# Performance work log

Measured on AMD Instinct MI355X. Metric: run time of the kernel, lower is better.

The kernel has to match this reference:

```python
import jax, jax.numpy as jnp
from jax import lax
import numpy as np
import math

B = 2; H = 64; W = 64; HW = H * W
CIN = 128; CH = 64          # in_chans, in_chans//2
E = 192; DEPTH = 2          # embed_dim, depth
DIN = 384; DST = 4; DTR = 12; KC = 4   # d_inner, d_state, dt_rank, d_conv
NC = 9
SAMPLE = HW // 2            # round(h*w*self_ratio), self_ratio=0.5
LE = HW - SAMPLE            # number of mask==0 (easy) tokens per row


def setup_inputs() -> dict:
    key = jax.random.key(0)
    ks = jax.random.split(key, 16)
    rn = lambda k, s, sc: jax.random.normal(k, s, jnp.float32) * sc
    return {
        'x': rn(ks[0], (B, CIN, H, W), 1.0),
        'head_id': 0,
        'sp_w': rn(ks[1], (1, CH, 1, 1), 1.0 / math.sqrt(CH)),
        'sp_b': jnp.zeros((1,), jnp.float32),
        'c0_w': rn(ks[2], (E, CIN, 1, 1), 1.0 / math.sqrt(CIN)),
        'c0_b': jnp.zeros((E,), jnp.float32),
        'blk_norm_w': jnp.ones((DEPTH, E), jnp.float32),
        'blk_conv_w': rn(ks[3], (DEPTH, E, E, 3, 3), 1.0 / math.sqrt(9 * E)),
        'blk_conv_b': jnp.zeros((DEPTH, E), jnp.float32),
        'm_in_w': rn(ks[4], (DEPTH, 2 * DIN, E), 1.0 / math.sqrt(E)),
        'm_conv_w': rn(ks[5], (DEPTH, DIN, KC), 1.0 / math.sqrt(KC)),
        'm_conv_b': jnp.zeros((DEPTH, DIN), jnp.float32),
        'm_x_w': rn(ks[6], (DEPTH, DTR + 2 * DST, DIN), 1.0 / math.sqrt(DIN)),
        'm_dt_w': rn(ks[7], (DEPTH, DIN, DTR), 1.0 / math.sqrt(DTR)),
        'm_dt_b': rn(ks[8], (DEPTH, DIN), 0.1),
        'm_Alog': jnp.tile(jnp.log(jnp.arange(1, DST + 1, dtype=jnp.float32)), (DEPTH, DIN, 1)),
        'm_D': jnp.ones((DEPTH, DIN), jnp.float32),
        'm_out_w': rn(ks[9], (DEPTH, E, DIN), 1.0 / math.sqrt(DIN)),
        'ln_w': jnp.ones((E,), jnp.float32),
        'ln_b': jnp.zeros((E,), jnp.float32),
        'h_conv_w': rn(ks[10], (E, E, 3, 3), 1.0 / math.sqrt(9 * E)),
        'h_bn_w': jnp.ones((E,), jnp.float32),
        'h_bn_b': jnp.zeros((E,), jnp.float32),
        'h_cls_w': rn(ks[11], (NC, E, 1, 1), 1.0 / math.sqrt(E)),
        'h_cls_b': jnp.zeros((NC,), jnp.float32),
    }


def conv2d(x, w, b=None, pad=0, dil=1):
    y = lax.conv_general_dilated(x, w, (1, 1), [(pad, pad), (pad, pad)],
                                 rhs_dilation=(dil, dil),
                                 dimension_numbers=('NCHW', 'OIHW', 'NCHW'))
    return y if b is None else y + b[None, :, None, None]


def silu(x):
    return x * jax.nn.sigmoid(x)


def mamba_mixer(xe, in_w, conv_w, conv_b, x_w, dt_w, dt_b, Alog, Dp, out_w):
    # xe: [B, L, E] easy tokens; standard Mamba selective scan (d_state=4, d_conv=4)
    Bn, L, _ = xe.shape
    xz = jnp.einsum('ble,de->bld', xe, in_w)          # [B,L,2*DIN]
    xh, z = jnp.split(xz, 2, axis=-1)
    xp = jnp.pad(xh, ((0, 0), (KC - 1, 0), (0, 0)))   # causal depthwise conv
    xc = conv_b + sum(conv_w[:, k] * xp[:, k:k + L, :] for k in range(KC))
    xc = silu(xc)
    dbl = jnp.einsum('bld,rd->blr', xc, x_w)
    dt, Bm, Cm = dbl[..., :DTR], dbl[..., DTR:DTR + DST], dbl[..., DTR + DST:]
    dt = jax.nn.softplus(jnp.einsum('blr,dr->bld', dt, dt_w) + dt_b)
    A = -jnp.exp(Alog)                                 # [DIN, DST]
    dA = jnp.exp(dt[..., None] * A)                    # [B,L,DIN,DST]
    dBx = dt[..., None] * Bm[:, :, None, :] * xc[..., None]

    def step(h, inp):
        dA_t, dBx_t, C_t = inp
        h = dA_t * h + dBx_t
        return h, jnp.einsum('bdn,bn->bd', h, C_t)

    h0 = jnp.zeros((Bn, DIN, DST), xe.dtype)
    _, ys = lax.scan(step, h0, (jnp.moveaxis(dA, 1, 0), jnp.moveaxis(dBx, 1, 0), jnp.moveaxis(Cm, 1, 0)))
    y = jnp.moveaxis(ys, 0, 1) + Dp * xc
    y = y * silu(z)
    return jnp.einsum('bld,ed->ble', y, out_w)


def snm_forward(x, sp_w, sp_b, c0_w, c0_b, blk_norm_w, blk_conv_w, blk_conv_b,
                m_in_w, m_conv_w, m_conv_b, m_x_w, m_dt_w, m_dt_b, m_Alog, m_D, m_out_w,
                ln_w, ln_b, h_conv_w, h_bn_w, h_bn_b, h_cls_w, h_cls_b):
    res, imgf = jnp.split(x, 2, axis=1)
    res = res * res                                    # prepocess_residual('square')
    simple_pred = jax.nn.sigmoid(conv2d(res, sp_w, sp_b))
    scores = (simple_pred + res.mean(1, keepdims=True)).reshape(B, HW)
    idx = jnp.argsort(scores, axis=1)[:, :SAMPLE]      # topk smallest
    feats = imgf.transpose(0, 2, 3, 1).reshape(B, HW, CH)

    def per_batch(f_i, idx_i):
        bank = f_i[idx_i]                              # [SAMPLE, CH]
        d2 = (jnp.sum(f_i * f_i, -1, keepdims=True)
              + jnp.sum(bank * bank, -1)[None, :]
              - 2.0 * f_i @ bank.T)
        d = jnp.sqrt(jnp.maximum(d2, 0.0))
        d = d.at[idx_i, jnp.arange(SAMPLE)].set(jnp.inf)   # exclude self matches
        nns = jnp.argmin(lax.stop_gradient(d), axis=1)
        return bank[nns] - f_i

    sres = jax.vmap(per_batch)(feats, idx)
    sres = sres.reshape(B, H, W, CH).transpose(0, 3, 1, 2)
    sres = sres * sres                                 # prepocess_residual('square')
    x2 = jnp.concatenate([res, sres], axis=1)          # [B, CIN, H, W]

    mask = jnp.zeros((B, HW), jnp.float32).at[jnp.arange(B)[:, None], idx].set(1.0)
    easy_idx = jnp.argsort(mask, axis=1)[:, :LE]       # stable: mask==0 positions in order
    bidx = jnp.arange(B)[:, None]

    fea = conv2d(x2, c0_w, c0_b)                       # [B,E,H,W]
    hidden = fea.reshape(B, E, HW).transpose(0, 2, 1)  # [B,L,E]
    residual = None
    for d in range(DEPTH):
        residual = hidden if residual is None else hidden + residual
        hid = residual * lax.rsqrt(jnp.mean(residual * residual, -1, keepdims=True) + 1e-5) * blk_norm_w[d]
        him = hid.transpose(0, 2, 1).reshape(B, E, H, W)
        him = conv2d(him, blk_conv_w[d], blk_conv_b[d], pad=1)
        hid = him.reshape(B, E, HW).transpose(0, 2, 1)
        easy = hid[bidx, easy_idx]                     # gather mask==0 tokens
        mixed = mamba_mixer(easy, m_in_w[d], m_conv_w[d], m_conv_b[d], m_x_w[d],
                            m_dt_w[d], m_dt_b[d], m_Alog[d], m_D[d], m_out_w[d])
        hidden = hid.at[bidx, easy_idx].set(mixed)     # scatter back

    out = hidden + residual
    mu = out.mean(-1, keepdims=True)
    var = jnp.mean((out - mu) ** 2, -1, keepdims=True)
    out = (out - mu) * lax.rsqrt(var + 1e-5) * ln_w + ln_b
    f = out.transpose(0, 2, 1).reshape(B, E, H, W)

    # head (atrous_rate=3): dilated conv (no bias) + BN(eval, running stats 0/1) + ReLU + 1x1
    h1 = conv2d(f, h_conv_w, pad=3, dil=3)
    bn_scale = h_bn_w / jnp.sqrt(1.0 + 1e-5)
    h1 = jax.nn.relu(h1 * bn_scale[None, :, None, None] + h_bn_b[None, :, None, None])
    logits = conv2d(h1, h_cls_w, h_cls_b)
    return simple_pred, logits


def reference(x, head_id, sp_w, sp_b, c0_w, c0_b, blk_norm_w, blk_conv_w, blk_conv_b,
              m_in_w, m_conv_w, m_conv_b, m_x_w, m_dt_w, m_dt_b, m_Alog, m_D, m_out_w,
              ln_w, ln_b, h_conv_w, h_bn_w, h_bn_b, h_cls_w, h_cls_b):
    # head_id=0 selects branch 0; only branch-0 params are materialized.
    return snm_forward(x, sp_w, sp_b, c0_w, c0_b, blk_norm_w, blk_conv_w, blk_conv_b,
                       m_in_w, m_conv_w, m_conv_b, m_x_w, m_dt_w, m_dt_b, m_Alog, m_D, m_out_w,
                       ln_w, ln_b, h_conv_w, h_bn_w, h_bn_b, h_cls_w, h_cls_b)
```

## Files before the change

kernel.cpp:

```cpp
#include <hip/hip_runtime.h>
#include <hip/hip_bf16.h>
#include <math.h>

#define BB 2
#define HWp 4096
#define CH 64
#define CIN 128
#define EE 192
#define DIN 384
#define DST 4
#define DTR 12
#define KC 4
#define NCc 9
#define SAMPLE 2048
#define LEc 2048
#define NCH 128
#define CLEN 16
#define NSPLIT 8
#define PADW 70
#define PADP 3

typedef __attribute__((ext_vector_type(8))) short bf16x8;
typedef __attribute__((ext_vector_type(4))) float f32x4;

__device__ __forceinline__ float sigmoid_fast(float x){ return 1.0f/(1.0f+__expf(-x)); }
__device__ __forceinline__ float softplus_f(float x){ return fmaxf(x,0.0f) + log1pf(expf(-fabsf(x))); }

__device__ __forceinline__ void split_bf16(float v, unsigned short& h, unsigned short& l){
  __hip_bfloat16 bh = __float2bfloat16(v);
  h = *(unsigned short*)&bh;
  float r = v - __bfloat162float(bh);
  __hip_bfloat16 bl = __float2bfloat16(r);
  l = *(unsigned short*)&bl;
}

#define SZ_WTBLK_BF (2*9*EE*EE)
#define SZ_WTHEAD_BF (9*EE*EE)
#define SZ_WTIN (2*EE*2*DIN)
#define SZ_WTOUT (2*DIN*EE)
#define SZ_WTC0 (CIN*EE)
#define SZ_WT_TOTAL (SZ_WTBLK_BF+SZ_WTHEAD_BF+SZ_WTIN+SZ_WTOUT+SZ_WTC0)
#define NXPI (BB*PADW*PADW*EE/2)
#define NRANKS (BB*HWp)

__global__ void prep_weights(const float* blk_w, const float* head_w, const float* in_w,
                             const float* out_w, const float* c0_w,
                             __hip_bfloat16* wtb_blk, __hip_bfloat16* wtb_head,
                             float* wt_in, float* wt_out, float* wt_c0,
                             int* xpad_i, int* ranks){
  int i = blockIdx.x*256 + threadIdx.x;
  if (i >= SZ_WT_TOTAL + NXPI + NRANKS) return;
  int o = i;
  if (o < SZ_WTBLK_BF){
    int j = o & 7;
    int lane = (o>>3) & 63;
    int nt = (o/512) % 3;
    int e = (o/1536) % 6;
    int tap = (o/9216) % 9;
    int eoB = (o/82944) % 4;
    int d = o / 331776;
    int m = lane & 15, kg = lane >> 4;
    int eo = eoB*48 + nt*16 + m;
    int ei = e*32 + kg*8 + j;
    wtb_blk[o] = __float2bfloat16(blk_w[(((d*EE+eo)*EE+ei)*9)+tap]);
    return;
  }
  o -= SZ_WTBLK_BF;
  if (o < SZ_WTHEAD_BF){
    int j = o & 7;
    int lane = (o>>3) & 63;
    int nt = (o/512) % 3;
    int e = (o/1536) % 6;
    int tap = (o/9216) % 9;
    int eoB = (o/82944) % 4;
    int m = lane & 15, kg = lane >> 4;
    int eo = eoB*48 + nt*16 + m;
    int ei = e*32 + kg*8 + j;
    wtb_head[o] = __float2bfloat16(head_w[((eo*EE+ei)*9)+tap]);
    return;
  }
  o -= SZ_WTHEAD_BF;
  if (o < SZ_WTIN){
    int dd = o % (2*DIN); int e = (o/(2*DIN))%EE; int d = o/(2*DIN*EE);
    wt_in[o] = in_w[((d*2*DIN)+dd)*EE + e]; return;
  }
  o -= SZ_WTIN;
  if (o < SZ_WTOUT){
    int eo = o%EE; int dch=(o/EE)%DIN; int d = o/(EE*DIN);
    wt_out[o] = out_w[((d*EE+eo)*DIN)+dch]; return;
  }
  o -= SZ_WTOUT;
  if (o < SZ_WTC0){
    int e = o%EE; int c = o/EE;  wt_c0[o] = c0_w[e*CIN + c]; return;
  }
  o -= SZ_WTC0;
  if (o < NXPI){ xpad_i[o] = 0; return; }
  o -= NXPI;
  ranks[o] = 0;
}

__global__ __launch_bounds__(256) void k_prep2(const float* __restrict__ x, const float* sp_w,
                       const float* sp_b, float* __restrict__ res2, float* __restrict__ feats,
                       unsigned short* __restrict__ fhi, unsigned short* __restrict__ flo,
                       float* scores, float* outSP){
  __shared__ float tile[CIN][33];
  int t = threadIdx.x;
  int p0 = blockIdx.x * 32;
  int b = p0 >> 12; int prow = p0 & 4095;
  const float* xb = x + (size_t)b*CIN*HWp + prow;
  #pragma unroll
  for (int i=0;i<4;i++){
    int idx = i*256 + t;
    int c = idx >> 3;
    int p4 = idx & 7;
    float4 v = *(const float4*)(xb + (size_t)c*HWp + p4*4);
    tile[c][p4*4+0]=v.x; tile[c][p4*4+1]=v.y; tile[c][p4*4+2]=v.z; tile[c][p4*4+3]=v.w;
  }
  __syncthreads();
  int lane = t & 63;
  int wv = t >> 6;
  float sw = sp_w[lane];
  float sb = sp_b[0];
  #pragma unroll
  for (int k=0;k<8;k++){
    int p = wv*8 + k;
    float v = tile[lane][p];
    float r2 = v*v;
    float f = tile[64+lane][p];
    int g = p0 + p;
    res2[(size_t)g*CH + lane] = r2;
    feats[(size_t)g*CH + lane] = f;
    unsigned short hh, ll;
    split_bf16(f, hh, ll);
    fhi[(size_t)g*CH + lane] = hh;
    flo[(size_t)g*CH + lane] = ll;
    float aS = r2*sw, aM = r2;
    #pragma unroll
    for (int msk=32; msk>0; msk>>=1){
      aS += __shfl_xor(aS, msk, 64);
      aM += __shfl_xor(aM, msk, 64);
    }
    if (lane == 0){
      float sp = 1.0f/(1.0f+expf(-(aS + sb)));
      outSP[g] = sp;
      scores[g] = sp + aM*(1.0f/CH);
    }
  }
}

__global__ void k_rank2(const float* scores, int* ranks){
  int b = blockIdx.z;
  int t = threadIdx.x;
  int p = blockIdx.x*256 + t;
  int j0 = blockIdx.y*256;
  __shared__ float s[256];
  s[t] = scores[b*HWp + j0 + t];
  float sp = scores[b*HWp + p];
  __syncthreads();
  int r = 0;
  #pragma unroll 8
  for (int jj=0;jj<256;jj++){
    float sj = s[jj];
    int j = j0 + jj;
    r += (sj < sp || (sj == sp && j < p)) ? 1 : 0;
  }
  atomicAdd(&ranks[b*HWp+p], r);
}

__global__ __launch_bounds__(1024) void k_easy(const int* ranks, int* idx_sorted, int* easy_idx){
  int b = blockIdx.x; int t = threadIdx.x;
  int lane = t & 63, wv = t >> 6;
  int i0 = t*4;
  int r0 = ranks[b*HWp+i0];
  int r1 = ranks[b*HWp+i0+1];
  int r2 = ranks[b*HWp+i0+2];
  int r3 = ranks[b*HWp+i0+3];
  int f0 = r0 >= SAMPLE, f1 = r1 >= SAMPLE, f2 = r2 >= SAMPLE, f3 = r3 >= SAMPLE;
  if (!f0) idx_sorted[b*SAMPLE + r0] = i0;
  if (!f1) idx_sorted[b*SAMPLE + r1] = i0+1;
  if (!f2) idx_sorted[b*SAMPLE + r2] = i0+2;
  if (!f3) idx_sorted[b*SAMPLE + r3] = i0+3;
  int cnt = f0+f1+f2+f3;
  int inc = cnt;
  #pragma unroll
  for (int off=1; off<64; off<<=1){
    int v = __shfl_up(inc, off, 64);
    if (lane >= off) inc += v;
  }
  __shared__ int wsum[16], woff[16];
  if (lane == 63) wsum[wv] = inc;
  __syncthreads();
  if (t == 0){
    int acc = 0;
    #pragma unroll
    for (int i=0;i<16;i++){ woff[i] = acc; acc += wsum[i]; }
  }
  __syncthreads();
  int pre = woff[wv] + inc - cnt;
  int base = b*LEc;
  if (f0) easy_idx[base+pre++] = i0;
  if (f1) easy_idx[base+pre++] = i0+1;
  if (f2) easy_idx[base+pre++] = i0+2;
  if (f3) easy_idx[base+pre]   = i0+3;
}

__global__ __launch_bounds__(64) void k_bank(const float* __restrict__ feats, const int* __restrict__ idx_sorted,
                       float* __restrict__ bnorm, unsigned short* __restrict__ bankhi,
                       unsigned short* __restrict__ banklo){
  int t = blockIdx.x*64+threadIdx.x;
  int b = t>>11;
  int row = idx_sorted[t];
  const float4* fr = (const float4*)(feats + (size_t)(b*HWp + row)*CH);
  ushort4* oh = (ushort4*)(bankhi + (size_t)t*CH);
  ushort4* ol = (ushort4*)(banklo + (size_t)t*CH);
  float s=0;
  #pragma unroll
  for (int k=0;k<16;k++){
    float4 v = fr[k];
    s += v.x*v.x+v.y*v.y+v.z*v.z+v.w*v.w;
    ushort4 h, l;
    split_bf16(v.x, h.x, l.x);
    split_bf16(v.y, h.y, l.y);
    split_bf16(v.z, h.z, l.z);
    split_bf16(v.w, h.w, l.w);
    oh[k] = h; ol[k] = l;
  }
  bnorm[t] = s;
}

__global__ __launch_bounds__(256) void k_nn_mfma(const unsigned short* __restrict__ fhi,
        const unsigned short* __restrict__ flo, const unsigned short* __restrict__ bankhi,
        const unsigned short* __restrict__ banklo, const float* __restrict__ bnorm,
        const int* __restrict__ idx_sorted, float* __restrict__ pval, int* __restrict__ pidx){
  int lane = threadIdx.x & 63;
  int wv = threadIdx.x >> 6;
  int m = lane & 15, kg = lane >> 4;
  int b = blockIdx.z;
  int qrel0 = blockIdx.x*64 + wv*16;
  int jsplit = blockIdx.y;
  const short* qh = (const short*)fhi + ((size_t)(b*HWp + qrel0 + m))*CH + kg*8;
  const short* ql = (const short*)flo + ((size_t)(b*HWp + qrel0 + m))*CH + kg*8;
  bf16x8 Ah0 = *(const bf16x8*)(qh);
  bf16x8 Ah1 = *(const bf16x8*)(qh + 32);
  bf16x8 Al0 = *(const bf16x8*)(ql);
  bf16x8 Al1 = *(const bf16x8*)(ql + 32);
  float best0=1e30f,best1=1e30f,best2=1e30f,best3=1e30f;
  int bj0=0,bj1=0,bj2=0,bj3=0;
  for (int jt=0; jt<16; jt++){
    int jb = jsplit*256 + jt*16;
    int j = jb + m;
    const short* bh = (const short*)bankhi + ((size_t)(b*SAMPLE + j))*CH + kg*8;
    const short* bl = (const short*)banklo + ((size_t)(b*SAMPLE + j))*CH + kg*8;
    bf16x8 Bh0 = *(const bf16x8*)(bh);
    bf16x8 Bh1 = *(const bf16x8*)(bh + 32);
    bf16x8 Bl0 = *(const bf16x8*)(bl);
    bf16x8 Bl1 = *(const bf16x8*)(bl + 32);
    f32x4 acc = {0,0,0,0};
    acc = __builtin_amdgcn_mfma_f32_16x16x32_bf16(Ah0, Bh0, acc, 0,0,0);
    acc = __builtin_amdgcn_mfma_f32_16x16x32_bf16(Ah1, Bh1, acc, 0,0,0);
    acc = __builtin_amdgcn_mfma_f32_16x16x32_bf16(Al0, Bh0, acc, 0,0,0);
    acc = __builtin_amdgcn_mfma_f32_16x16x32_bf16(Al1, Bh1, acc, 0,0,0);
    acc = __builtin_amdgcn_mfma_f32_16x16x32_bf16(Ah0, Bl0, acc, 0,0,0);
    acc = __builtin_amdgcn_mfma_f32_16x16x32_bf16(Ah1, Bl1, acc, 0,0,0);
    acc = __builtin_amdgcn_mfma_f32_16x16x32_bf16(Al0, Bl0, acc, 0,0,0);
    acc = __builtin_amdgcn_mfma_f32_16x16x32_bf16(Al1, Bl1, acc, 0,0,0);
    float bn = bnorm[b*SAMPLE + j];
    int src = idx_sorted[b*SAMPLE + j];
    float v0 = bn - 2.0f*acc[0];
    float v1 = bn - 2.0f*acc[1];
    float v2 = bn - 2.0f*acc[2];
    float v3 = bn - 2.0f*acc[3];
    int qp = qrel0 + kg*4;
    if (src != qp   && v0 < best0){ best0 = v0; bj0 = j; }
    if (src != qp+1 && v1 < best1){ best1 = v1; bj1 = j; }
    if (src != qp+2 && v2 < best2){ best2 = v2; bj2 = j; }
    if (src != qp+3 && v3 < best3){ best3 = v3; bj3 = j; }
  }
  #pragma unroll
  for (int mask=1; mask<16; mask<<=1){
    float ov; int oj;
    ov = __shfl_xor(best0, mask, 64); oj = __shfl_xor(bj0, mask, 64);
    if (ov < best0 || (ov == best0 && oj < bj0)){ best0 = ov; bj0 = oj; }
    ov = __shfl_xor(best1, mask, 64); oj = __shfl_xor(bj1, mask, 64);
    if (ov < best1 || (ov == best1 && oj < bj1)){ best1 = ov; bj1 = oj; }
    ov = __shfl_xor(best2, mask, 64); oj = __shfl_xor(bj2, mask, 64);
    if (ov < best2 || (ov == best2 && oj < bj2)){ best2 = ov; bj2 = oj; }
    ov = __shfl_xor(best3, mask, 64); oj = __shfl_xor(bj3, mask, 64);
    if (ov < best3 || (ov == best3 && oj < bj3)){ best3 = ov; bj3 = oj; }
  }
  if (m == 0){
    int qg = b*HWp + qrel0 + kg*4;
    pval[(qg+0)*NSPLIT + jsplit] = best0; pidx[(qg+0)*NSPLIT + jsplit] = bj0;
    pval[(qg+1)*NSPLIT + jsplit] = best1; pidx[(qg+1)*NSPLIT + jsplit] = bj1;
    pval[(qg+2)*NSPLIT + jsplit] = best2; pidx[(qg+2)*NSPLIT + jsplit] = bj2;
    pval[(qg+3)*NSPLIT + jsplit] = best3; pidx[(qg+3)*NSPLIT + jsplit] = bj3;
  }
}

__global__ __launch_bounds__(192) void k_c0(const float* res2, const float* __restrict__ feats,
                                            const int* idx_sorted, const float* pval, const int* pidx,
                                            const float* wt_c0, const float* c0_b, float* hidden){
  __shared__ float xin[CIN][20];
  __shared__ int brow[16];
  int base = blockIdx.x * 16;
  int b = base >> 12;
  int t = threadIdx.x;
  if (t < 16){
    int q = base + t;
    float best = 1e30f; int bj = 0;
    #pragma unroll
    for (int s=0;s<NSPLIT;s++){
      float v = pval[q*NSPLIT+s]; int j = pidx[q*NSPLIT+s];
      if (v < best){ best = v; bj = j; }
    }
    brow[t] = idx_sorted[b*SAMPLE + bj];
  }
  __syncthreads();
  for (int i=t; i<16*CIN; i+=192){
    int px = i >> 7, c = i & 127;
    float v;
    if (c < CH) v = res2[(size_t)(base+px)*CH + c];
    else {
      int cc = c - CH;
      float a = feats[(size_t)(b*HWp + brow[px])*CH + cc];
      float f = feats[(size_t)(base+px)*CH + cc];
      float d = a - f; v = d*d;
    }
    xin[c][px] = v;
  }
  __syncthreads();
  int e = t;
  float bias = c0_b[e];
  float acc[16];
  #pragma unroll
  for (int px=0;px<16;px++) acc[px]=bias;
  for (int c=0;c<CIN;c++){
    float w = wt_c0[c*EE + e];
    const float4* vr = (const float4*)(&xin[c][0]);
    float4 v0=vr[0], v1=vr[1], v2=vr[2], v3=vr[3];
    acc[0]+=v0.x*w; acc[1]+=v0.y*w; acc[2]+=v0.z*w; acc[3]+=v0.w*w;
    acc[4]+=v1.x*w; acc[5]+=v1.y*w; acc[6]+=v1.z*w; acc[7]+=v1.w*w;
    acc[8]+=v2.x*w; acc[9]+=v2.y*w; acc[10]+=v2.z*w; acc[11]+=v2.w*w;
    acc[12]+=v3.x*w; acc[13]+=v3.y*w; acc[14]+=v3.z*w; acc[15]+=v3.w*w;
  }
  #pragma unroll
  for (int px=0;px<16;px++) hidden[(size_t)(base+px)*EE + e] = acc[px];
}

__global__ __launch_bounds__(192) void k_rms(const float* hidden, float* residual,
                                             __hip_bfloat16* __restrict__ xpad,
                                             const float* norm_w, int first){
  int row = blockIdx.x; int e = threadIdx.x;
  int o = row*EE + e;
  float h = hidden[o];
  float r = first ? h : (h + residual[o]);
  residual[o] = r;
  float s = r*r;
  #pragma unroll
  for (int m=32;m>0;m>>=1) s += __shfl_xor(s, m, 64);
  __shared__ float red[3];
  if ((e&63)==0) red[e>>6] = s;
  __syncthreads();
  float tot = red[0]+red[1]+red[2];
  float rms = rsqrtf(tot*(1.0f/EE) + 1e-5f);
  int b = row >> 12; int p = row & 4095; int y = p >> 6; int x = p & 63;
  xpad[((size_t)(b*PADW + y + PADP)*PADW + (x + PADP))*EE + e] = __float2bfloat16(r*rms*norm_w[e]);
}

template<int DIL, int FUSE>
__global__ __launch_bounds__(256,3) void k_conv3s(const __hip_bfloat16* __restrict__ xp,
        const __hip_bfloat16* __restrict__ wt, const float* __restrict__ bias,
        const float* __restrict__ bnw, const float* __restrict__ bnb,
        float* __restrict__ out){
  __shared__ short wlds[2][9216];
  int t = threadIdx.x;
  int lane = t & 63;
  int wv = t >> 6;
  int m = lane & 15, kg = lane >> 4;
  int rb = blockIdx.x;
  int b = rb >> 6, y = rb & 63;
  int eoB = blockIdx.y;
  int x = wv*16 + m;
  const short* xs = (const short*)xp;
  const short* ws = (const short*)wt + (size_t)eoB * 82944;
  int aBase0 = ((b*PADW + y + PADP)*PADW + (x + PADP))*EE + kg*8;

  f32x4 acc0={0,0,0,0}, acc1={0,0,0,0}, acc2={0,0,0,0};

  {
    const ushort4* src = (const ushort4*)(ws);
    ushort4* dst = (ushort4*)(&wlds[0][0]);
    #pragma unroll
    for (int k=0;k<9;k++) dst[k*256+t] = src[k*256+t];
  }
  bf16x8 curA[6];
  {
    int aB = aBase0 + ((-1)*DIL*PADW + (-1)*DIL)*EE;
    #pragma unroll
    for (int e=0;e<6;e++) curA[e] = *(const bf16x8*)(xs + aB + e*32);
  }
  __syncthreads();

  for (int tap=0; tap<9; tap++){
    int cur = tap & 1;
    ushort4 nxtW[9];
    bf16x8 nxtA[6];
    if (tap < 8){
      const ushort4* src = (const ushort4*)(ws + (size_t)(tap+1)*9216);
      #pragma unroll
      for (int k=0;k<9;k++) nxtW[k] = src[k*256+t];
      int ky = (tap+1)/3, kx = (tap+1)%3;
      int aB = aBase0 + ((ky-1)*DIL*PADW + (kx-1)*DIL)*EE;
      #pragma unroll
      for (int e=0;e<6;e++) nxtA[e] = *(const bf16x8*)(xs + aB + e*32);
    }
    const short* bl = &wlds[cur][0];
    #pragma unroll
    for (int e=0;e<6;e++){
      bf16x8 b0 = *(const bf16x8*)(bl + (e*3+0)*512 + lane*8);
      bf16x8 b1 = *(const bf16x8*)(bl + (e*3+1)*512 + lane*8);
      bf16x8 b2 = *(const bf16x8*)(bl + (e*3+2)*512 + lane*8);
      acc0 = __builtin_amdgcn_mfma_f32_16x16x32_bf16(curA[e], b0, acc0, 0,0,0);
      acc1 = __builtin_amdgcn_mfma_f32_16x16x32_bf16(curA[e], b1, acc1, 0,0,0);
      acc2 = __builtin_amdgcn_mfma_f32_16x16x32_bf16(curA[e], b2, acc2, 0,0,0);
    }
    if (tap < 8){
      ushort4* dst = (ushort4*)(&wlds[cur^1][0]);
      #pragma unroll
      for (int k=0;k<9;k++) dst[k*256+t] = nxtW[k];
      #pragma unroll
      for (int e=0;e<6;e++) curA[e] = nxtA[e];
    }
    __syncthreads();
  }

  int px0 = y*64 + wv*16 + kg*4;
  #pragma unroll
  for (int nt=0; nt<3; nt++){
    f32x4 a = (nt==0)?acc0:((nt==1)?acc1:acc2);
    int eo = eoB*48 + nt*16 + m;
    float add=0.0f, scale=0.0f, sh=0.0f;
    if (FUSE){ scale = bnw[eo]*rsqrtf(1.0f+1e-5f); sh = bnb[eo]; }
    else add = bias[eo];
    #pragma unroll
    for (int r=0;r<4;r++){
      float v = a[r];
      if (FUSE) v = fmaxf(v*scale + sh, 0.0f);
      else v += add;
      out[((size_t)(b*HWp) + px0 + r)*EE + eo] = v;
    }
  }
}

__global__ __launch_bounds__(256) void k_inproj(const float* hid2, const int* easy_idx, const float* wt_in_d,
                                                float* xh, float* zb){
  __shared__ float sh[EE][12];
  int bid = blockIdx.x;
  int b = bid >> 8; int l0 = (bid & 255)*8;
  int t = threadIdx.x;
  for (int i=t; i<8*EE; i+=256){
    int l = i/EE; int e = i - l*EE;
    int row = easy_idx[b*LEc + l0 + l];
    sh[e][l] = hid2[(size_t)(b*HWp + row)*EE + e];
  }
  __syncthreads();
  float acc0[8], acc1[8], acc2[8];
  #pragma unroll
  for (int l=0;l<8;l++){ acc0[l]=0; acc1[l]=0; acc2[l]=0; }
  for (int e=0;e<EE;e++){
    float w0 = wt_in_d[e*768 + t];
    float w1 = wt_in_d[e*768 + t + 256];
    float w2 = wt_in_d[e*768 + t + 512];
    const float4* vr = (const float4*)(&sh[e][0]);
    float4 a = vr[0], c = vr[1];
    float v[8] = {a.x,a.y,a.z,a.w,c.x,c.y,c.z,c.w};
    #pragma unroll
    for (int l=0;l<8;l++){ acc0[l]+=v[l]*w0; acc1[l]+=v[l]*w1; acc2[l]+=v[l]*w2; }
  }
  #pragma unroll
  for (int k=0;k<3;k++){
    int dd = t + k*256;
    #pragma unroll
    for (int l=0;l<8;l++){
      float o = (k==0)?acc0[l]:((k==1)?acc1[l]:acc2[l]);
      int rb = b*LEc + l0 + l;
      if (dd < DIN) xh[rb*DIN + dd] = o;
      else zb[rb*DIN + dd - DIN] = o;
    }
  }
}

__global__ __launch_bounds__(128) void k_mpre(const float* xh, const float* cw, const float* cb,
                                              const float* xw, const float* dtw, const float* dtb_w,
                                              float* xc, float* bc, float* dtb){
  int row = blockIdx.x;
  int l = row & 2047;
  int t = threadIdx.x;
  __shared__ float sxc[DIN];
  __shared__ float sdbl[20];
  for (int i=t; i<DIN; i+=128){
    const float* w = cw + i*KC;
    float s = cb[i];
    #pragma unroll
    for (int k=0;k<KC;k++){
      int ls = l - 3 + k;
      if (ls >= 0) s += w[k]*xh[(row-3+k)*DIN + i];
    }
    s = s * sigmoid_fast(s);
    sxc[i] = s;
    xc[row*DIN+i] = s;
  }
  __syncthreads();
  if (t < 20){
    const float* w = xw + t*DIN;
    float a=0,b2=0,c=0,d2=0;
    for (int i=0;i<DIN;i+=4){ a+=sxc[i]*w[i]; b2+=sxc[i+1]*w[i+1]; c+=sxc[i+2]*w[i+2]; d2+=sxc[i+3]*w[i+3]; }
    float o = a+b2+c+d2;
    sdbl[t] = o;
    if (t >= DTR) bc[row*8 + (t-DTR)] = o;
  }
  __syncthreads();
  for (int i=t; i<DIN; i+=128){
    const float* w = dtw + i*DTR;
    float s = dtb_w[i];
    #pragma unroll
    for (int k=0;k<DTR;k++) s += sdbl[k]*w[k];
    dtb[row*DIN+i] = softplus_f(s);
  }
}

__global__ void k_scanA(const float* dt, const float* xc, const float* bc, const float* Alog, float* chnk){
  int g = blockIdx.x*256+threadIdx.x;
  int dch = g % DIN; int c = (g/DIN) % NCH; int b = g/(DIN*NCH);
  float A[4], P[4]={1,1,1,1}, h[4]={0,0,0,0};
  #pragma unroll
  for (int n=0;n<4;n++) A[n] = -__expf(Alog[dch*DST+n]);
  int lbase = b*LEc + c*CLEN;
  for (int s=0;s<CLEN;s++){
    int base = lbase + s;
    float dtv = dt[base*DIN + dch];
    float xcv = xc[base*DIN + dch];
    float dx = dtv*xcv;
    #pragma unroll
    for (int n=0;n<4;n++){
      float dA = __expf(dtv*A[n]);
      float Bn = bc[base*8 + n];
      h[n] = dA*h[n] + dx*Bn;
      P[n] *= dA;
    }
  }
  float* o = chnk + (size_t)g*8;
  #pragma unroll
  for (int n=0;n<4;n++){ o[n]=P[n]; o[4+n]=h[n]; }
}

__global__ void k_scanB(const float* chnk, float* hin){
  int g = blockIdx.x*256+threadIdx.x;
  if (g >= BB*DIN) return;
  int dch = g % DIN; int b = g / DIN;
  float h0=0,h1=0,h2=0,h3=0;
  for (int cb=0; cb<NCH/8; cb++){
    float4 P[8], Hl[8];
    #pragma unroll
    for (int u=0;u<8;u++){
      const float4* cp = (const float4*)(chnk + (size_t)((b*NCH + cb*8+u)*DIN + dch)*8);
      P[u] = cp[0]; Hl[u] = cp[1];
    }
    #pragma unroll
    for (int u=0;u<8;u++){
      int idx = (b*NCH + cb*8+u)*DIN + dch;
      float4 hv; hv.x=h0; hv.y=h1; hv.z=h2; hv.w=h3;
      *(float4*)(hin + (size_t)idx*4) = hv;
      h0 = P[u].x*h0 + Hl[u].x;
      h1 = P[u].y*h1 + Hl[u].y;
      h2 = P[u].z*h2 + Hl[u].z;
      h3 = P[u].w*h3 + Hl[u].w;
    }
  }
}

__global__ void k_scanC(const float* dt, const float* xc, const float* zb, const float* bc, const float* Alog,
                        const float* Dw, const float* hin, float* yb){
  int g = blockIdx.x*256+threadIdx.x;
  int dch = g % DIN; int c = (g/DIN) % NCH; int b = g/(DIN*NCH);
  float A[4], h[4];
  #pragma unroll
  for (int n=0;n<4;n++){ A[n] = -__expf(Alog[dch*DST+n]); h[n] = hin[(size_t)g*4+n]; }
  float Dv = Dw[dch];
  int lbase = b*LEc + c*CLEN;
  for (int s=0;s<CLEN;s++){
    int base = lbase + s;
    float dtv = dt[base*DIN+dch];
    float xcv = xc[base*DIN+dch];
    float zv  = zb[base*DIN+dch];
    float dx = dtv*xcv;
    float y = 0.0f;
    #pragma unroll
    for (int n=0;n<4;n++){
      float dA = __expf(dtv*A[n]);
      h[n] = dA*h[n] + dx*bc[base*8+n];
      y += h[n]*bc[base*8+4+n];
    }
    y = (y + Dv*xcv) * (zv * sigmoid_fast(zv));
    yb[base*DIN + dch] = y;
  }
}

__global__ __launch_bounds__(192) void k_outproj(const float* yb, const int* easy_idx, const float* wt_out_d,
                                                 float* hidden){
  __shared__ float sy[DIN][20];
  int bid = blockIdx.x; int b = bid >> 7; int l0 = (bid & 127)*16;
  int t = threadIdx.x;
  for (int i=t; i<16*DIN; i+=192){
    int l = i/DIN; int c = i - l*DIN;
    sy[c][l] = yb[(b*LEc + l0 + l)*DIN + c];
  }
  __syncthreads();
  float acc[16];
  #pragma unroll
  for (int l=0;l<16;l++) acc[l]=0;
  for (int c=0;c<DIN;c++){
    float w = wt_out_d[c*EE + t];
    const float4* vr = (const float4*)(&sy[c][0]);
    float4 a=vr[0], b4=vr[1], c4=vr[2], d4=vr[3];
    acc[0]+=a.x*w;  acc[1]+=a.y*w;  acc[2]+=a.z*w;  acc[3]+=a.w*w;
    acc[4]+=b4.x*w; acc[5]+=b4.y*w; acc[6]+=b4.z*w; acc[7]+=b4.w*w;
    acc[8]+=c4.x*w; acc[9]+=c4.y*w; acc[10]+=c4.z*w; acc[11]+=c4.w*w;
    acc[12]+=d4.x*w; acc[13]+=d4.y*w; acc[14]+=d4.z*w; acc[15]+=d4.w*w;
  }
  #pragma unroll
  for (int l=0;l<16;l++){
    int row = easy_idx[b*LEc + l0 + l];
    hidden[(size_t)(b*HWp + row)*EE + t] = acc[l];
  }
}

__global__ __launch_bounds__(192) void k_ln(const float* hidden, const float* residual,
                                            const float* lnw, const float* lnb,
                                            __hip_bfloat16* __restrict__ xpad){
  int row = blockIdx.x; int e = threadIdx.x;
  int o = row*EE + e;
  float v = hidden[o] + residual[o];
  __shared__ float redA[3], redB[3];
  float s = v;
  #pragma unroll
  for (int m=32;m>0;m>>=1) s += __shfl_xor(s, m, 64);
  if ((e&63)==0) redA[e>>6] = s;
  __syncthreads();
  float mu = (redA[0]+redA[1]+redA[2])*(1.0f/EE);
  float dv = v - mu;
  float s2 = dv*dv;
  #pragma unroll
  for (int m=32;m>0;m>>=1) s2 += __shfl_xor(s2, m, 64);
  if ((e&63)==0) redB[e>>6] = s2;
  __syncthreads();
  float var = (redB[0]+redB[1]+redB[2])*(1.0f/EE);
  float o2 = dv*rsqrtf(var + 1e-5f)*lnw[e] + lnb[e];
  int b = row >> 12; int p = row & 4095; int y = p >> 6; int x = p & 63;
  xpad[((size_t)(b*PADW + y + PADP)*PADW + (x + PADP))*EE + e] = __float2bfloat16(o2);
}

__global__ __launch_bounds__(64) void k_cls(const float* h1, const float* cls_w, const float* cls_b, float* out){
  __shared__ float wsm[NCc][EE];
  int t = threadIdx.x;
  for (int i=t; i<NCc*EE; i+=64){ wsm[i/EE][i%EE] = cls_w[i]; }
  __syncthreads();
  int g = blockIdx.x*64 + t;
  int p = g & 4095; int b = g >> 12;
  const float4* hrow = (const float4*)(h1 + (size_t)g*EE);
  float acc[NCc];
  #pragma unroll
  for (int n=0;n<NCc;n++) acc[n] = cls_b[n];
  for (int c4=0;c4<EE/4;c4++){
    float4 h = hrow[c4];
    #pragma unroll
    for (int n=0;n<NCc;n++){
      const float4 wv = *(const float4*)(&wsm[n][c4*4]);
      acc[n] += h.x*wv.x + h.y*wv.y + h.z*wv.z + h.w*wv.w;
    }
  }
  #pragma unroll
  for (int n=0;n<NCc;n++)
    out[((size_t)b*NCc + n)*HWp + p] = acc[n];
}

extern "C" void kernel_launch(void* const* d_in, const int* in_sizes, int n_in,
                              void* d_out, int out_size, void* d_ws, size_t ws_size,
                              hipStream_t stream) {
  const float* x          = (const float*)d_in[0];
  const float* sp_w       = (const float*)d_in[2];
  const float* sp_b       = (const float*)d_in[3];
  const float* c0_w       = (const float*)d_in[4];
  const float* c0_b       = (const float*)d_in[5];
  const float* blk_norm_w = (const float*)d_in[6];
  const float* blk_conv_w = (const float*)d_in[7];
  const float* blk_conv_b = (const float*)d_in[8];
  const float* m_in_w     = (const float*)d_in[9];
  const float* m_conv_w   = (const float*)d_in[10];
  const float* m_conv_b   = (const float*)d_in[11];
  const float* m_x_w      = (const float*)d_in[12];
  const float* m_dt_w     = (const float*)d_in[13];
  const float* m_dt_b     = (const float*)d_in[14];
  const float* m_Alog     = (const float*)d_in[15];
  const float* m_D        = (const float*)d_in[16];
  const float* m_out_w    = (const float*)d_in[17];
  const float* ln_w       = (const float*)d_in[18];
  const float* ln_b       = (const float*)d_in[19];
  const float* h_conv_w   = (const float*)d_in[20];
  const float* h_bn_w     = (const float*)d_in[21];
  const float* h_bn_b     = (const float*)d_in[22];
  const float* h_cls_w    = (const float*)d_in[23];
  const float* h_cls_b    = (const float*)d_in[24];

  float* out_sp     = (float*)d_out;
  float* out_logits = (float*)d_out + BB*HWp;

  float* w = (float*)d_ws;
  size_t off = 0;
  auto alloc = [&](size_t n){ float* p = w + off; off += (n + 63) & ~size_t(63); return p; };
  float* res2    = alloc(BB*HWp*CH);
  float* feats   = alloc(BB*HWp*CH);
  float* scores  = alloc(BB*HWp);
  float* bnorm   = alloc(BB*SAMPLE);
  float* hidden  = alloc(BB*HWp*EE);
  float* residual= alloc(BB*HWp*EE);
  float* hid2    = alloc(BB*HWp*EE);
  float* xh      = alloc(BB*LEc*DIN);
  float* zb      = alloc(BB*LEc*DIN);
  float* xc      = alloc(BB*LEc*DIN);
  float* dtb     = alloc(BB*LEc*DIN);
  float* yb      = alloc(BB*LEc*DIN);
  float* bcbuf   = alloc(BB*LEc*8);
  float* pval    = alloc(BB*HWp*NSPLIT);
  float* chnk    = alloc((size_t)BB*NCH*DIN*8);
  float* hin     = alloc((size_t)BB*NCH*DIN*4);
  float* wt_in   = alloc(SZ_WTIN);
  float* wt_out  = alloc(SZ_WTOUT);
  float* wt_c0   = alloc(SZ_WTC0);
  __hip_bfloat16* wtb_blk  = (__hip_bfloat16*)alloc(SZ_WTBLK_BF/2);
  __hip_bfloat16* wtb_head = (__hip_bfloat16*)alloc(SZ_WTHEAD_BF/2);
  __hip_bfloat16* xpad     = (__hip_bfloat16*)alloc(BB*PADW*PADW*EE/2);
  unsigned short* fhi    = (unsigned short*)alloc(BB*HWp*CH/2);
  unsigned short* flo    = (unsigned short*)alloc(BB*HWp*CH/2);
  unsigned short* bankhi = (unsigned short*)alloc(BB*SAMPLE*CH/2);
  unsigned short* banklo = (unsigned short*)alloc(BB*SAMPLE*CH/2);
  int* pidx       = (int*)alloc(BB*HWp*NSPLIT);
  int* idx_sorted = (int*)alloc(BB*SAMPLE);
  int* ranks      = (int*)alloc(BB*HWp);
  int* easy_idx   = (int*)alloc(BB*LEc);
  if (off*sizeof(float) > ws_size) return;

  prep_weights<<<(SZ_WT_TOTAL+NXPI+NRANKS+255)/256, 256, 0, stream>>>(
      blk_conv_w, h_conv_w, m_in_w, m_out_w, c0_w,
      wtb_blk, wtb_head, wt_in, wt_out, wt_c0, (int*)xpad, ranks);
  k_prep2<<<BB*HWp/32, 256, 0, stream>>>(x, sp_w, sp_b, res2, feats, fhi, flo, scores, out_sp);
  k_rank2<<<dim3(16,16,BB), 256, 0, stream>>>(scores, ranks);
  k_easy<<<BB, 1024, 0, stream>>>(ranks, idx_sorted, easy_idx);
  k_bank<<<BB*SAMPLE/64, 64, 0, stream>>>(feats, idx_sorted, bnorm, bankhi, banklo);
  k_nn_mfma<<<dim3(HWp/64, NSPLIT, BB), 256, 0, stream>>>(fhi, flo, bankhi, banklo, bnorm,
                                                          idx_sorted, pval, pidx);
  k_c0<<<BB*HWp/16, 192, 0, stream>>>(res2, feats, idx_sorted, pval, pidx, wt_c0, c0_b, hidden);

  for (int d=0; d<2; d++){
    k_rms<<<BB*HWp, 192, 0, stream>>>(hidden, residual, xpad, blk_norm_w + d*EE, d==0);
    k_conv3s<1,0><<<dim3(BB*64,4), 256, 0, stream>>>(xpad, wtb_blk + d*9*EE*EE,
                                                     blk_conv_b + d*EE, nullptr, nullptr, hidden);
    k_inproj<<<BB*(LEc/8), 256, 0, stream>>>(hidden, easy_idx, wt_in + d*EE*2*DIN, xh, zb);
    k_mpre<<<BB*LEc, 128, 0, stream>>>(xh, m_conv_w + d*DIN*KC, m_conv_b + d*DIN,
                                       m_x_w + d*(DTR+2*DST)*DIN, m_dt_w + d*DIN*DTR, m_dt_b + d*DIN,
                                       xc, bcbuf, dtb);
    k_scanA<<<BB*NCH*DIN/256, 256, 0, stream>>>(dtb, xc, bcbuf, m_Alog + d*DIN*DST, chnk);
    k_scanB<<<(BB*DIN+255)/256, 256, 0, stream>>>(chnk, hin);
    k_scanC<<<BB*NCH*DIN/256, 256, 0, stream>>>(dtb, xc, zb, bcbuf, m_Alog + d*DIN*DST,
                                                m_D + d*DIN, hin, yb);
    k_outproj<<<BB*(LEc/16), 192, 0, stream>>>(yb, easy_idx, wt_out + d*DIN*EE, hidden);
  }

  k_ln<<<BB*HWp, 192, 0, stream>>>(hidden, residual, ln_w, ln_b, xpad);
  k_conv3s<3,1><<<dim3(BB*64,4), 256, 0, stream>>>(xpad, wtb_head, nullptr, h_bn_w, h_bn_b, hid2);
  k_cls<<<BB*HWp/64, 64, 0, stream>>>(hid2, h_cls_w, h_cls_b, out_logits);
}
```

Before: 421.0 us.

## Use split-bf16 MFMA for in_proj and fuse three scan kernels into one

The in_proj GEMM now uses bf16 hi/lo split MFMA (four products per k-step) with weights pre-packed into the MFMA fragment layout in prep_weights, replacing the FP32 shared-memory FMA loop. The three-pass chunked selective scan is merged into one kernel: each block handles one channel, each of 128 threads scans a 16-step chunk, and thread 0 combines the chunk carries serially in shared memory. This removes two launches and the global round-trips for the chunk carries. The cost is a serial 128-step loop on a single thread and lower memory coalescing, since each block reads only one channel stride.

```diff
diff --git a/kernel.cpp b/kernel.cpp
--- a/kernel.cpp
+++ b/kernel.cpp
@@ -46,7 +46,8 @@
 __global__ void prep_weights(const float* blk_w, const float* head_w, const float* in_w,
                              const float* out_w, const float* c0_w,
                              __hip_bfloat16* wtb_blk, __hip_bfloat16* wtb_head,
-                             float* wt_in, float* wt_out, float* wt_c0,
+                             unsigned short* wtb_in_hi, unsigned short* wtb_in_lo,
+                             float* wt_out, float* wt_c0,
                              int* xpad_i, int* ranks){
   int i = blockIdx.x*256 + threadIdx.x;
   if (i >= SZ_WT_TOTAL + NXPI + NRANKS) return;
@@ -81,8 +82,18 @@
   }
   o -= SZ_WTHEAD_BF;
   if (o < SZ_WTIN){
-    int dd = o % (2*DIN); int e = (o/(2*DIN))%EE; int d = o/(2*DIN*EE);
-    wt_in[o] = in_w[((d*2*DIN)+dd)*EE + e]; return;
+    int j = o & 7;
+    int lane = (o>>3) & 63;
+    int ks = (o/512) % 6;
+    int nt = (o/3072) % 48;
+    int d = o / 147456;
+    int m = lane & 15, kg = lane >> 4;
+    int dd = nt*16 + m;
+    int ei = ks*32 + kg*8 + j;
+    float v = in_w[((size_t)(d*768)+dd)*EE + ei];
+    unsigned short hh, ll; split_bf16(v, hh, ll);
+    wtb_in_hi[o] = hh; wtb_in_lo[o] = ll;
+    return;
   }
   o -= SZ_WTIN;
   if (o < SZ_WTOUT){
@@ -452,40 +463,50 @@
   }
 }
 
-__global__ __launch_bounds__(256) void k_inproj(const float* hid2, const int* easy_idx, const float* wt_in_d,
-                                                float* xh, float* zb){
-  __shared__ float sh[EE][12];
+__global__ __launch_bounds__(256) void k_inproj(const float* __restrict__ hid, const int* easy_idx,
+        const unsigned short* __restrict__ wthi, const unsigned short* __restrict__ wtlo,
+        float* __restrict__ xh, float* __restrict__ zb){
+  int lane = threadIdx.x & 63, wv = threadIdx.x >> 6;
+  int m = lane & 15, kg = lane >> 4;
   int bid = blockIdx.x;
-  int b = bid >> 8; int l0 = (bid & 255)*8;
-  int t = threadIdx.x;
-  for (int i=t; i<8*EE; i+=256){
-    int l = i/EE; int e = i - l*EE;
-    int row = easy_idx[b*LEc + l0 + l];
-    sh[e][l] = hid2[(size_t)(b*HWp + row)*EE + e];
-  }
-  __syncthreads();
-  float acc0[8], acc1[8], acc2[8];
-  #pragma unroll
-  for (int l=0;l<8;l++){ acc0[l]=0; acc1[l]=0; acc2[l]=0; }
-  for (int e=0;e<EE;e++){
-    float w0 = wt_in_d[e*768 + t];
-    float w1 = wt_in_d[e*768 + t + 256];
-    float w2 = wt_in_d[e*768 + t + 512];
-    const float4* vr = (const float4*)(&sh[e][0]);
-    float4 a = vr[0], c = vr[1];
-    float v[8] = {a.x,a.y,a.z,a.w,c.x,c.y,c.z,c.w};
-    #pragma unroll
-    for (int l=0;l<8;l++){ acc0[l]+=v[l]*w0; acc1[l]+=v[l]*w1; acc2[l]+=v[l]*w2; }
-  }
-  #pragma unroll
-  for (int k=0;k<3;k++){
-    int dd = t + k*256;
-    #pragma unroll
-    for (int l=0;l<8;l++){
-      float o = (k==0)?acc0[l]:((k==1)?acc1[l]:acc2[l]);
-      int rb = b*LEc + l0 + l;
-      if (dd < DIN) xh[rb*DIN + dd] = o;
-      else zb[rb*DIN + dd - DIN] = o;
+  int b = bid >> 5; int l0 = (bid & 31)*64 + wv*16;
+  int nq = blockIdx.y;
+  int row = easy_idx[b*LEc + l0 + m];
+  const float* srcp = hid + (size_t)(b*HWp + row)*EE + kg*8;
+  bf16x8 Ah[6], Al[6];
+  #pragma unroll
+  for (int ks=0; ks<6; ks++){
+    const float* sp = srcp + ks*32;
+    #pragma unroll
+    for (int q=0;q<8;q++){
+      float v = sp[q];
+      unsigned short hh, ll; split_bf16(v, hh, ll);
+      Ah[ks][q] = (short)hh; Al[ks][q] = (short)ll;
+    }
+  }
+  const short* wh = (const short*)wthi;
+  const short* wl = (const short*)wtlo;
+  for (int ntile=0; ntile<12; ntile++){
+    int nt = nq*12 + ntile;
+    const short* ph = wh + (size_t)nt*3072 + lane*8;
+    const short* pl = wl + (size_t)nt*3072 + lane*8;
+    f32x4 acc = {0,0,0,0};
+    #pragma unroll
+    for (int ks=0; ks<6; ks++){
+      bf16x8 Bh = *(const bf16x8*)(ph + ks*512);
+      bf16x8 Bl = *(const bf16x8*)(pl + ks*512);
+      acc = __builtin_amdgcn_mfma_f32_16x16x32_bf16(Ah[ks], Bh, acc, 0,0,0);
+      acc = __builtin_amdgcn_mfma_f32_16x16x32_bf16(Al[ks], Bh, acc, 0,0,0);
+      acc = __builtin_amdgcn_mfma_f32_16x16x32_bf16(Ah[ks], Bl, acc, 0,0,0);
+      acc = __builtin_amdgcn_mfma_f32_16x16x32_bf16(Al[ks], Bl, acc, 0,0,0);
+    }
+    int dd = nt*16 + m;
+    #pragma unroll
+    for (int r=0;r<4;r++){
+      int rb = b*LEc + l0 + kg*4 + r;
+      float o = acc[r];
+      if (dd < DIN) xh[(size_t)rb*DIN + dd] = o;
+      else zb[(size_t)rb*DIN + (dd-DIN)] = o;
     }
   }
 }
@@ -529,13 +550,16 @@
   }
 }
 
-__global__ void k_scanA(const float* dt, const float* xc, const float* bc, const float* Alog, float* chnk){
-  int g = blockIdx.x*256+threadIdx.x;
-  int dch = g % DIN; int c = (g/DIN) % NCH; int b = g/(DIN*NCH);
-  float A[4], P[4]={1,1,1,1}, h[4]={0,0,0,0};
+__global__ __launch_bounds__(128) void k_scan(const float* dt, const float* xc, const float* zb,
+        const float* bc, const float* Alog, const float* Dw, float* yb){
+  int blk = blockIdx.x;
+  int dch = blk % DIN; int b = blk / DIN;
+  int t = threadIdx.x;
+  float A[4];
   #pragma unroll
   for (int n=0;n<4;n++) A[n] = -__expf(Alog[dch*DST+n]);
-  int lbase = b*LEc + c*CLEN;
+  int lbase = b*LEc + t*CLEN;
+  float P[4]={1,1,1,1}, h[4]={0,0,0,0};
   for (int s=0;s<CLEN;s++){
     int base = lbase + s;
     float dtv = dt[base*DIN + dch];
@@ -549,45 +573,22 @@
       P[n] *= dA;
     }
   }
-  float* o = chnk + (size_t)g*8;
-  #pragma unroll
-  for (int n=0;n<4;n++){ o[n]=P[n]; o[4+n]=h[n]; }
-}
-
-__global__ void k_scanB(const float* chnk, float* hin){
-  int g = blockIdx.x*256+threadIdx.x;
-  if (g >= BB*DIN) return;
-  int dch = g % DIN; int b = g / DIN;
-  float h0=0,h1=0,h2=0,h3=0;
-  for (int cb=0; cb<NCH/8; cb++){
-    float4 P[8], Hl[8];
-    #pragma unroll
-    for (int u=0;u<8;u++){
-      const float4* cp = (const float4*)(chnk + (size_t)((b*NCH + cb*8+u)*DIN + dch)*8);
-      P[u] = cp[0]; Hl[u] = cp[1];
-    }
-    #pragma unroll
-    for (int u=0;u<8;u++){
-      int idx = (b*NCH + cb*8+u)*DIN + dch;
-      float4 hv; hv.x=h0; hv.y=h1; hv.z=h2; hv.w=h3;
-      *(float4*)(hin + (size_t)idx*4) = hv;
-      h0 = P[u].x*h0 + Hl[u].x;
-      h1 = P[u].y*h1 + Hl[u].y;
-      h2 = P[u].z*h2 + Hl[u].z;
-      h3 = P[u].w*h3 + Hl[u].w;
-    }
-  }
-}
-
-__global__ void k_scanC(const float* dt, const float* xc, const float* zb, const float* bc, const float* Alog,
-                        const float* Dw, const float* hin, float* yb){
-  int g = blockIdx.x*256+threadIdx.x;
-  int dch = g % DIN; int c = (g/DIN) % NCH; int b = g/(DIN*NCH);
-  float A[4], h[4];
-  #pragma unroll
-  for (int n=0;n<4;n++){ A[n] = -__expf(Alog[dch*DST+n]); h[n] = hin[(size_t)g*4+n]; }
+  __shared__ float sP[128][4], sH[128][4], s0[128][4];
+  #pragma unroll
+  for (int n=0;n<4;n++){ sP[t][n]=P[n]; sH[t][n]=h[n]; }
+  __syncthreads();
+  if (t == 0){
+    float hh[4]={0,0,0,0};
+    for (int c=0;c<128;c++){
+      #pragma unroll
+      for (int n=0;n<4;n++){ s0[c][n]=hh[n]; hh[n]=sP[c][n]*hh[n]+sH[c][n]; }
+    }
+  }
+  __syncthreads();
+  float hc[4];
+  #pragma unroll
+  for (int n=0;n<4;n++) hc[n]=s0[t][n];
   float Dv = Dw[dch];
-  int lbase = b*LEc + c*CLEN;
   for (int s=0;s<CLEN;s++){
     int base = lbase + s;
     float dtv = dt[base*DIN+dch];
@@ -598,8 +599,8 @@
     #pragma unroll
     for (int n=0;n<4;n++){
       float dA = __expf(dtv*A[n]);
-      h[n] = dA*h[n] + dx*bc[base*8+n];
-      y += h[n]*bc[base*8+4+n];
+      hc[n] = dA*hc[n] + dx*bc[base*8+n];
+      y += hc[n]*bc[base*8+4+n];
     }
     y = (y + Dv*xcv) * (zv * sigmoid_fast(zv));
     yb[base*DIN + dch] = y;
@@ -732,13 +733,12 @@
   float* yb      = alloc(BB*LEc*DIN);
   float* bcbuf   = alloc(BB*LEc*8);
   float* pval    = alloc(BB*HWp*NSPLIT);
-  float* chnk    = alloc((size_t)BB*NCH*DIN*8);
-  float* hin     = alloc((size_t)BB*NCH*DIN*4);
-  float* wt_in   = alloc(SZ_WTIN);
   float* wt_out  = alloc(SZ_WTOUT);
   float* wt_c0   = alloc(SZ_WTC0);
   __hip_bfloat16* wtb_blk  = (__hip_bfloat16*)alloc(SZ_WTBLK_BF/2);
   __hip_bfloat16* wtb_head = (__hip_bfloat16*)alloc(SZ_WTHEAD_BF/2);
+  unsigned short* wtb_in_hi = (unsigned short*)alloc(SZ_WTIN/2);
+  unsigned short* wtb_in_lo = (unsigned short*)alloc(SZ_WTIN/2);
   __hip_bfloat16* xpad     = (__hip_bfloat16*)alloc(BB*PADW*PADW*EE/2);
   unsigned short* fhi    = (unsigned short*)alloc(BB*HWp*CH/2);
   unsigned short* flo    = (unsigned short*)alloc(BB*HWp*CH/2);
@@ -752,7 +752,7 @@
 
   prep_weights<<<(SZ_WT_TOTAL+NXPI+NRANKS+255)/256, 256, 0, stream>>>(
       blk_conv_w, h_conv_w, m_in_w, m_out_w, c0_w,
-      wtb_blk, wtb_head, wt_in, wt_out, wt_c0, (int*)xpad, ranks);
+      wtb_blk, wtb_head, wtb_in_hi, wtb_in_lo, wt_out, wt_c0, (int*)xpad, ranks);
   k_prep2<<<BB*HWp/32, 256, 0, stream>>>(x, sp_w, sp_b, res2, feats, fhi, flo, scores, out_sp);
   k_rank2<<<dim3(16,16,BB), 256, 0, stream>>>(scores, ranks);
   k_easy<<<BB, 1024, 0, stream>>>(ranks, idx_sorted, easy_idx);
@@ -765,14 +765,13 @@
     k_rms<<<BB*HWp, 192, 0, stream>>>(hidden, residual, xpad, blk_norm_w + d*EE, d==0);
     k_conv3s<1,0><<<dim3(BB*64,4), 256, 0, stream>>>(xpad, wtb_blk + d*9*EE*EE,
                                                      blk_conv_b + d*EE, nullptr, nullptr, hidden);
-    k_inproj<<<BB*(LEc/8), 256, 0, stream>>>(hidden, easy_idx, wt_in + d*EE*2*DIN, xh, zb);
+    k_inproj<<<dim3(BB*LEc/64, 4), 256, 0, stream>>>(hidden, easy_idx,
+                                                     wtb_in_hi + (size_t)d*147456,
+                                                     wtb_in_lo + (size_t)d*147456, xh, zb);
     k_mpre<<<BB*LEc, 128, 0, stream>>>(xh, m_conv_w + d*DIN*KC, m_conv_b + d*DIN,
                                        m_x_w + d*(DTR+2*DST)*DIN, m_dt_w + d*DIN*DTR, m_dt_b + d*DIN,
                                        xc, bcbuf, dtb);
-    k_scanA<<<BB*NCH*DIN/256, 256, 0, stream>>>(dtb, xc, bcbuf, m_Alog + d*DIN*DST, chnk);
-    k_scanB<<<(BB*DIN+255)/256, 256, 0, stream>>>(chnk, hin);
-    k_scanC<<<BB*NCH*DIN/256, 256, 0, stream>>>(dtb, xc, zb, bcbuf, m_Alog + d*DIN*DST,
-                                                m_D + d*DIN, hin, yb);
+    k_scan<<<BB*DIN, 128, 0, stream>>>(dtb, xc, zb, bcbuf, m_Alog + d*DIN*DST, m_D + d*DIN, yb);
     k_outproj<<<BB*(LEc/16), 192, 0, stream>>>(yb, easy_idx, wt_out + d*DIN*EE, hidden);
   }
 
```

After: 482.3 us. +14.6%, slower.
